# Kernel tuning notes

Hardware: AMD Instinct MI355X
Metric: run time of the kernel (lower is better)

The kernel has to match this reference:

```python
import jax, jax.numpy as jnp
import numpy as np

N_NODES = 51200      # 128 graphs * 400 ROIs
N_ROI = 400
HID = 64             # 'batch_size' arg of the torch module = hidden channels = n_timepoints
N_EDGES = 1638400    # avg degree 32
N_CLASSES = 2
NEG_SLOPE = 0.01


def setup_inputs():
    key = jax.random.key(0)
    ks = jax.random.split(key, 20)
    s = 0.05
    inp = {
        'x': jax.random.normal(ks[0], (N_NODES, HID), dtype=jnp.float32),
        'edge_index': jax.random.randint(ks[1], (2, N_EDGES), 0, N_NODES, dtype=jnp.int64),
        'edge_weight': jax.random.uniform(ks[2], (N_EDGES,), dtype=jnp.float32),
        # GCNConv weights stored [in, out]; biases [out]
        'W1': jax.random.normal(ks[3], (HID, HID), dtype=jnp.float32) * s,
        'b1': jnp.zeros((HID,), jnp.float32),
        'W2': jax.random.normal(ks[4], (HID, HID), dtype=jnp.float32) * s,
        'b2': jnp.zeros((HID,), jnp.float32),
        'W3': jax.random.normal(ks[5], (HID, HID), dtype=jnp.float32) * s,
        'b3': jnp.zeros((HID,), jnp.float32),
        'W4': jax.random.normal(ks[6], (HID, HID), dtype=jnp.float32) * s,
        'b4': jnp.zeros((HID,), jnp.float32),
        'fc1_w': jax.random.normal(ks[7], (N_ROI * HID, 256), dtype=jnp.float32) * 0.01,
        'fc1_b': jnp.zeros((256,), jnp.float32),
        'fc2_w': jax.random.normal(ks[8], (256, 128), dtype=jnp.float32) * s,
        'fc2_b': jnp.zeros((128,), jnp.float32),
        'fc3_w': jax.random.normal(ks[9], (128, N_CLASSES), dtype=jnp.float32) * s,
        'fc3_b': jnp.zeros((N_CLASSES,), jnp.float32),
    }
    return inp


def _gcn_norm(edge_index, edge_weight, n):
    # PyG GCNConv: add self-loops (weight 1), symmetric D^-1/2 A D^-1/2 normalization
    loop = jnp.arange(n, dtype=edge_index.dtype)
    src = jnp.concatenate([edge_index[0], loop])
    dst = jnp.concatenate([edge_index[1], loop])
    w = jnp.concatenate([edge_weight, jnp.ones((n,), edge_weight.dtype)])
    deg = jax.ops.segment_sum(w, dst, num_segments=n)
    dis = jnp.where(deg > 0, jax.lax.rsqrt(jnp.maximum(deg, 1e-30)), 0.0)
    norm = dis[src] * w * dis[dst]
    return src, dst, norm


def _conv(h, W, b, src, dst, norm, n):
    h = h @ W                                   # [N, out]
    msg = h[src] * norm[:, None]                # gather + scale
    out = jax.ops.segment_sum(msg, dst, num_segments=n) + b
    return out


def _leaky(v):
    return jnp.where(v >= 0, v, NEG_SLOPE * v)


def _head(h, fc1_w, fc1_b, fc2_w, fc2_b, fc3_w, fc3_b):
    # global_mean_pool with batch = arange(N) is identity; pool == reshape to graphs
    g = h.reshape(-1, N_ROI * HID)              # [G, n_roi*hid]
    g = g @ fc1_w + fc1_b                       # dropout is eval-mode identity
    g = g @ fc2_w + fc2_b
    g = g @ fc3_w + fc3_b
    return g


def reference(x, edge_index, edge_weight, W1, b1, W2, b2, W3, b3, W4, b4,
              fc1_w, fc1_b, fc2_w, fc2_b, fc3_w, fc3_b):
    n = x.shape[0]
    src, dst, norm = _gcn_norm(edge_index, edge_weight, n)
    h = _leaky(_conv(x, W1, b1, src, dst, norm, n))
    h = _leaky(_conv(h, W2, b2, src, dst, norm, n))
    h = _leaky(_conv(h, W3, b3, src, dst, norm, n))
    h = _leaky(_conv(h, W4, b4, src, dst, norm, n))
    logits = _head(h, fc1_w, fc1_b, fc2_w, fc2_b, fc3_w, fc3_b)
    logits0 = _head(x, fc1_w, fc1_b, fc2_w, fc2_b, fc3_w, fc3_b)
    penal = 0.09 * logits.shape[0] / jnp.linalg.norm(logits - logits0)
    return logits, penal
```

## Files before the change

kernel.cpp:

```cpp
#include <hip/hip_runtime.h>
#include <cstddef>

#define N_NODES 51200
#define N_EDGES 1638400
#define HID 64
#define N_ROI 400
#define N_GRAPHS 128
#define KHEAD 25600
#define NEG_SLOPE 0.01f
#define CAP 80
#define NCHUNK 400
#define CHUNK 4096
#define NBIN 512
#define BINSZ 100
#define LSTRIDE 81

typedef unsigned short u16;
typedef unsigned int u32;
typedef unsigned char u8;
typedef float f32x2 __attribute__((ext_vector_type(2)));

__device__ inline u16 f2bf(float f) {
    u32 u = __float_as_uint(f);
    u32 r = u + 0x7FFFu + ((u >> 16) & 1u);
    return (u16)(r >> 16);
}
__device__ inline float bf2f(u16 h) { return __uint_as_float(((u32)h) << 16); }

__device__ inline f32x2 dec8lo(u32 v) { return __builtin_amdgcn_cvt_pk_f32_fp8((int)v, false); }
__device__ inline f32x2 dec8hi(u32 v) { return __builtin_amdgcn_cvt_pk_f32_fp8((int)v, true); }
template <bool HI>
__device__ inline u32 enc8(float a, float b, u32 old) {
    return (u32)__builtin_amdgcn_cvt_pk_fp8_f32(a, b, (int)old, HI);
}
__device__ inline u32 pack4_fp8(float a, float b, float c, float d) {
    u32 w = enc8<false>(a, b, 0u);
    return enc8<true>(c, d, w);
}


__global__ __launch_bounds__(1024) void k1(const int* __restrict__ ei,
                                           const float* __restrict__ ew,
                                           uint2* __restrict__ chunkData,
                                           u32* __restrict__ offcnt,
                                           const float* __restrict__ x,
                                           u8* __restrict__ x8,
                                           const float* __restrict__ fc2w,
                                           const float* __restrict__ fc3w,
                                           const float* __restrict__ fc1b,
                                           const float* __restrict__ fc2b,
                                           const float* __restrict__ fc3b,
                                           float* __restrict__ fc23,
                                           float* __restrict__ bc) {
    int bid = blockIdx.x, t = threadIdx.x;
    __shared__ u32 cnt[NBIN];
    __shared__ u32 scan[NBIN];
    __shared__ u32 cur[NBIN];
    __shared__ uint2 stag[CHUNK];
    __shared__ float t1[128];

    if (bid < NCHUNK) {
        if (t < NBIN) cnt[t] = 0;
        __syncthreads();
        int base = bid * CHUNK;
        u32 lo[4]; float wv[4]; int bin[4];
        #pragma unroll
        for (int i = 0; i < 4; i++) {
            int e = base + i * 1024 + t;
            int s = ei[e], d = ei[N_EDGES + e];
            wv[i] = ew[e];
            bin[i] = d / BINSZ;
            lo[i] = (u32)s | ((u32)(d - bin[i] * BINSZ) << 16);
            atomicAdd(&cnt[bin[i]], 1u);
        }
        __syncthreads();
        if (t < NBIN) scan[t] = cnt[t];
        __syncthreads();
        for (int off = 1; off < NBIN; off <<= 1) {
            u32 add = (t < NBIN && t >= off) ? scan[t - off] : 0u;
            __syncthreads();
            if (t < NBIN) scan[t] += add;
            __syncthreads();
        }
        if (t < NBIN) cur[t] = scan[t] - cnt[t];
        __syncthreads();
        if (t < NBIN) offcnt[(size_t)bid * NBIN + t] = cur[t] | (cnt[t] << 16);
        __syncthreads();
        #pragma unroll
        for (int i = 0; i < 4; i++) {
            u32 pos = atomicAdd(&cur[bin[i]], 1u);
            stag[pos] = make_uint2(lo[i], __float_as_uint(wv[i]));
        }
        __syncthreads();
        #pragma unroll
        for (int i = 0; i < 4; i++)
            chunkData[base + i * 1024 + t] = stag[i * 1024 + t];
    } else if (bid < 600) {
        int idx = (bid - NCHUNK) * 1024 + t;
        const float4* xp = reinterpret_cast<const float4*>(x) + (size_t)idx * 4;
        float4 a = xp[0], b = xp[1], c = xp[2], d = xp[3];
        reinterpret_cast<uint4*>(x8)[idx] =
            make_uint4(pack4_fp8(a.x, a.y, a.z, a.w), pack4_fp8(b.x, b.y, b.z, b.w),
                       pack4_fp8(c.x, c.y, c.z, c.w), pack4_fp8(d.x, d.y, d.z, d.w));
    } else {
        if (t < 256) {
            float s0 = 0.f, s1 = 0.f;
            const float* row = fc2w + t * 128;
            for (int j = 0; j < 128; j++) {
                float a = row[j];
                s0 += a * fc3w[2 * j];
                s1 += a * fc3w[2 * j + 1];
            }
            fc23[2 * t] = s0;
            fc23[2 * t + 1] = s1;
        }
        if (t < 128) {
            float s = fc2b[t];
            for (int k = 0; k < 256; k++) s += fc1b[k] * fc2w[k * 128 + t];
            t1[t] = s;
        }
        __syncthreads();
        if (t < 2) {
            float s = fc3b[t];
            for (int j = 0; j < 128; j++) s += t1[j] * fc3w[2 * j + t];
            bc[t] = s;
        }
    }
}


__global__ __launch_bounds__(256) void k1t(const u32* __restrict__ in,
                                           u32* __restrict__ outT) {
    __shared__ u32 tile[32][33];
    int cx = blockIdx.x % 13, by = blockIdx.x / 13;
    int c0 = cx * 32, b0 = by * 32;
    int tx = threadIdx.x & 31, ty = threadIdx.x >> 5;
    for (int i = ty; i < 32; i += 8) {
        int c = c0 + i;
        if (c < NCHUNK) tile[i][tx] = in[(size_t)c * NBIN + b0 + tx];
    }
    __syncthreads();
    for (int i = ty; i < 32; i += 8) {
        int b = b0 + i;
        int c = c0 + tx;
        if (c < NCHUNK) outT[(size_t)b * NCHUNK + c] = tile[tx][i];
    }
}


__global__ __launch_bounds__(512) void k2(const uint2* __restrict__ chunkData,
                                          const u32* __restrict__ offcntT,
                                          u32* __restrict__ buck,
                                          int* __restrict__ cnts,
                                          float* __restrict__ dis,
                                          const float* __restrict__ fc1w,
                                          const float* __restrict__ fc23,
                                          float* __restrict__ Wc) {
    int bid = blockIdx.x, t = threadIdx.x;
    __shared__ u32 lbuck[BINSZ * LSTRIDE];
    __shared__ u32 lcnt[BINSZ];
    __shared__ float ldeg[BINSZ];
    __shared__ u32 oc[NCHUNK];

    if (bid < NBIN) {
        if (t < BINSZ) { lcnt[t] = 0; ldeg[t] = 0.f; }
        if (t < NCHUNK) oc[t] = offcntT[(size_t)bid * NCHUNK + t];
        __syncthreads();
        int w = t >> 6, lane = t & 63;
        int sBase = w * 50;
        for (int j = 0; j < 56; j += 8) {
            int s = sBase + j + (lane >> 3);
            int i0 = lane & 7;
            int k = 0, off = 0;
            if (j + (lane >> 3) < 50) {
                u32 o = oc[s];
                off = (int)(o & 0xffffu);
                k = (int)(o >> 16);
            }
            const uint2* cd = chunkData + (size_t)s * CHUNK + off;
            for (int i = i0; i < k; i += 8) {
                uint2 e = cd[i];
                u32 node = e.x >> 16;
                u32 src = e.x & 0xffffu;
                float ww = __uint_as_float(e.y);
                u32 pos = atomicAdd(&lcnt[node], 1u);
                if (pos < CAP - 1) lbuck[node * LSTRIDE + pos] = ((u32)f2bf(ww) << 16) | src;
                atomicAdd(&ldeg[node], ww);
            }
        }
        __syncthreads();
        int sg = t >> 5, ln = t & 31;
        for (int n = sg; n < BINSZ; n += 16) {
            int node = bid * BINSZ + n;
            int k = min((int)lcnt[n], CAP - 1);
            u32* dst = buck + (size_t)node * CAP;
            for (int i = ln; i < k; i += 32) dst[i] = lbuck[n * LSTRIDE + i];
            if (ln == 0) {
                cnts[node] = k;
                dis[node] = rsqrtf(1.f + ldeg[n]);
            }
        }
    } else {
        float* f23 = (float*)lbuck;
        f23[t] = fc23[t];
        __syncthreads();
        int r = (bid - NBIN) * 512 + t;
        const float* row = fc1w + (size_t)r * 256;
        float s0 = 0.f, s1 = 0.f;
        #pragma unroll 8
        for (int k = 0; k < 256; k++) {
            float a = row[k];
            s0 += a * f23[2 * k];
            s1 += a * f23[2 * k + 1];
        }
        Wc[2 * r] = s0;
        Wc[2 * r + 1] = s1;
    }
}


__global__ __launch_bounds__(1024) void k3(u32* __restrict__ buck,
                                           int* __restrict__ cnts,
                                           const float* __restrict__ dis) {
    int gt = blockIdx.x * 1024 + threadIdx.x;
    int node = gt >> 5, sub = gt & 31;
    float d = dis[node];
    int k = cnts[node];
    u32* bk = buck + (size_t)node * CAP;
    for (int j = sub; j < k; j += 32) {
        u32 e = bk[j];
        float val = bf2f((u16)(e >> 16)) * d * dis[e & 0xffffu];
        bk[j] = ((u32)f2bf(val) << 16) | (e & 0xffffu);
    }
    if (sub == 0) {
        bk[k] = ((u32)f2bf(d * d) << 16) | (u32)node;
        cnts[node] = k + 1;
    }
}


__global__ __launch_bounds__(512) void k_layer(const u8* __restrict__ H8,
                                               const u32* __restrict__ buck,
                                               const int* __restrict__ cnts,
                                               const float* __restrict__ W,
                                               const float* __restrict__ bias,
                                               u8* __restrict__ Hout) {
    __shared__ float Ws[64][64];
    __shared__ float ZsT[64][33];
    int t = threadIdx.x;
    int base = blockIdx.x * 32;

    #pragma unroll
    for (int i = 0; i < 2; i++) {
        int f = t + i * 512;
        int kk = f >> 4, c4 = f & 15;
        float4 wv = reinterpret_cast<const float4*>(W)[f];
        *reinterpret_cast<float4*>(&Ws[kk][c4 * 4]) = wv;
    }

    int grp = t >> 4, sub = t & 15;
    int node = base + grp;
    int k = cnts[node];
    const u32* bk = buck + (size_t)node * CAP;
    const u8* Hb = H8 + sub * 4;
    float a0 = 0.f, a1 = 0.f, a2 = 0.f, a3 = 0.f;
    for (int j0 = 0; j0 < k; j0 += 16) {
        int idx = j0 + sub;
        u32 pre = (idx < k) ? bk[idx] : 0u;
        #pragma unroll
        for (int i = 0; i < 16; i++) {
            u32 e = (u32)__shfl((int)pre, i, 16);
            float val = __uint_as_float(e & 0xffff0000u);
            u32 src = e & 0xffffu;
            u32 r = *reinterpret_cast<const u32*>(Hb + (size_t)src * HID);
            f32x2 lo = dec8lo(r), hi = dec8hi(r);
            a0 += val * lo.x; a1 += val * lo.y;
            a2 += val * hi.x; a3 += val * hi.y;
        }
    }
    ZsT[4 * sub + 0][grp] = a0;
    ZsT[4 * sub + 1][grp] = a1;
    ZsT[4 * sub + 2][grp] = a2;
    ZsT[4 * sub + 3][grp] = a3;
    __syncthreads();

    int r = t >> 4, c4 = t & 15;
    float4 acc = {0.f, 0.f, 0.f, 0.f};
    #pragma unroll 8
    for (int kk = 0; kk < 64; kk++) {
        float a = ZsT[kk][r];
        const float4 w = *reinterpret_cast<const float4*>(&Ws[kk][c4 * 4]);
        acc.x += a * w.x; acc.y += a * w.y; acc.z += a * w.z; acc.w += a * w.w;
    }
    float4 bb = reinterpret_cast<const float4*>(bias)[c4];
    float v0 = acc.x + bb.x, v1 = acc.y + bb.y, v2 = acc.z + bb.z, v3 = acc.w + bb.w;
    v0 = v0 >= 0.f ? v0 : NEG_SLOPE * v0;
    v1 = v1 >= 0.f ? v1 : NEG_SLOPE * v1;
    v2 = v2 >= 0.f ? v2 : NEG_SLOPE * v2;
    v3 = v3 >= 0.f ? v3 : NEG_SLOPE * v3;
    *reinterpret_cast<u32*>(Hout + (size_t)(base + r) * HID + c4 * 4) =
        pack4_fp8(v0, v1, v2, v3);
}


__global__ __launch_bounds__(256) void k_logits(const u8* __restrict__ h4,
                                                const float* __restrict__ x,
                                                const float* __restrict__ Wc,
                                                const float* __restrict__ bc,
                                                float* __restrict__ out,
                                                float* __restrict__ sq,
                                                int* __restrict__ done) {
    int g = blockIdx.x, t = threadIdx.x;
    const u8* bh = h4 + (size_t)g * KHEAD;
    const float* bx = x + (size_t)g * KHEAD;
    float aH0 = 0.f, aH1 = 0.f, aX0 = 0.f, aX1 = 0.f;
    for (int k2 = t; k2 < KHEAD / 2; k2 += 256) {
        u32 hv = reinterpret_cast<const u16*>(bh)[k2];
        f32x2 h = dec8lo(hv);
        float2 xv = reinterpret_cast<const float2*>(bx)[k2];
        float4 wc = reinterpret_cast<const float4*>(Wc)[k2];
        aH0 += h.x * wc.x + h.y * wc.z;
        aH1 += h.x * wc.y + h.y * wc.w;
        aX0 += xv.x * wc.x + xv.y * wc.z;
        aX1 += xv.x * wc.y + xv.y * wc.w;
    }
    for (int off = 32; off > 0; off >>= 1) {
        aH0 += __shfl_down(aH0, off);
        aH1 += __shfl_down(aH1, off);
        aX0 += __shfl_down(aX0, off);
        aX1 += __shfl_down(aX1, off);
    }
    __shared__ float red[4][4];
    int wave = t >> 6, lane = t & 63;
    if (lane == 0) {
        red[wave][0] = aH0; red[wave][1] = aH1;
        red[wave][2] = aX0; red[wave][3] = aX1;
    }
    __syncthreads();
    if (t == 0) {
        float h0 = red[0][0] + red[1][0] + red[2][0] + red[3][0];
        float h1 = red[0][1] + red[1][1] + red[2][1] + red[3][1];
        float x0 = red[0][2] + red[1][2] + red[2][2] + red[3][2];
        float x1 = red[0][3] + red[1][3] + red[2][3] + red[3][3];
        out[2 * g]     = h0 + bc[0];
        out[2 * g + 1] = h1 + bc[1];
        float d0 = h0 - x0, d1 = h1 - x1;
        atomicAdd(sq, d0 * d0 + d1 * d1);
        __threadfence();
        int c = atomicAdd(done, 1);
        if (c == N_GRAPHS - 1) {
            __threadfence();
            float s = atomicAdd(sq, 0.f);
            out[2 * N_GRAPHS] = 0.09f * (float)N_GRAPHS / sqrtf(s);
        }
    }
}


extern "C" void kernel_launch(void* const* d_in, const int* in_sizes, int n_in,
                              void* d_out, int out_size, void* d_ws, size_t ws_size,
                              hipStream_t stream) {
    const float* x    = (const float*)d_in[0];
    const int*   ei   = (const int*)d_in[1];
    const float* ew   = (const float*)d_in[2];
    const float* W1   = (const float*)d_in[3];
    const float* b1   = (const float*)d_in[4];
    const float* W2   = (const float*)d_in[5];
    const float* b2   = (const float*)d_in[6];
    const float* W3   = (const float*)d_in[7];
    const float* b3   = (const float*)d_in[8];
    const float* W4   = (const float*)d_in[9];
    const float* b4   = (const float*)d_in[10];
    const float* fc1w = (const float*)d_in[11];
    const float* fc1b = (const float*)d_in[12];
    const float* fc2w = (const float*)d_in[13];
    const float* fc2b = (const float*)d_in[14];
    const float* fc3w = (const float*)d_in[15];
    const float* fc3b = (const float*)d_in[16];
    float* out = (float*)d_out;

    char* base = (char*)d_ws;
    size_t off = 0;
    auto alloc = [&](size_t bytes) -> void* {
        void* p = base + off;
        off += (bytes + 255) & ~(size_t)255;
        return p;
    };
    uint2* chunkData = (uint2*)alloc((size_t)N_EDGES * 8);
    u32*   offcnt    = (u32*)alloc((size_t)NCHUNK * NBIN * 4);
    u32*   offcntT   = (u32*)alloc((size_t)NCHUNK * NBIN * 4);
    u32*   buck      = (u32*)alloc((size_t)N_NODES * CAP * 4);
    int*   cnts      = (int*)alloc((size_t)N_NODES * 4);
    float* dis       = (float*)alloc((size_t)N_NODES * 4);
    u8*    x8        = (u8*)alloc((size_t)N_NODES * HID);
    u8*    ha        = (u8*)alloc((size_t)N_NODES * HID);
    u8*    hb        = (u8*)alloc((size_t)N_NODES * HID);
    float* fc23      = (float*)alloc(512 * 4);
    float* bc        = (float*)alloc(2 * 4);
    float* Wc        = (float*)alloc((size_t)KHEAD * 2 * 4);
    char*  ctrl      = (char*)alloc(256);
    float* sq        = (float*)ctrl;
    int*   done      = (int*)(ctrl + 4);

    (void)hipMemsetAsync(ctrl, 0, 8, stream);
    k1<<<601, 1024, 0, stream>>>(ei, ew, chunkData, offcnt, x, x8,
                                 fc2w, fc3w, fc1b, fc2b, fc3b, fc23, bc);
    k1t<<<13 * 16, 256, 0, stream>>>(offcnt, offcntT);
    k2<<<NBIN + 50, 512, 0, stream>>>(chunkData, offcntT, buck, cnts, dis,
                                      fc1w, fc23, Wc);
    k3<<<1600, 1024, 0, stream>>>(buck, cnts, dis);

    const float* Wl[4] = {W1, W2, W3, W4};
    const float* bl[4] = {b1, b2, b3, b4};
    u8* hbufs[2] = {ha, hb};
    const u8* hin = x8;
    for (int l = 0; l < 4; l++) {
        u8* hout = hbufs[l & 1];
        k_layer<<<N_NODES / 32, 512, 0, stream>>>(hin, buck, cnts,
                                                  Wl[l], bl[l], hout);
        hin = hout;
    }

    k_logits<<<N_GRAPHS, 256, 0, stream>>>(hin, x, Wc, bc, out, sq, done);
}
```

Measured before the change: 192.1 us.

## Fold edge normalization into layer kernel, vectorize binning, and retile GEMM

Removes the k3 normalization pass: each layer now applies dis[src] and dis[dst] on the fly and handles the self-loop from the node's own features. Chunk size doubles with vectorized int4/float4 edge loads, and the per-chunk scan now uses wave shuffles instead of a barrier-heavy Hillis-Steele loop. The layer kernel processes 64 nodes per 1024-thread block with a 4x4 register-tiled 64x64 GEMM run by 256 threads. The trade-off is one extra dis gather per edge in each of the four layers, and idle threads during the GEMM phase.

```diff
diff --git a/kernel.cpp b/kernel.cpp
--- a/kernel.cpp
+++ b/kernel.cpp
@@ -9,8 +9,8 @@
 #define KHEAD 25600
 #define NEG_SLOPE 0.01f
 #define CAP 80
-#define NCHUNK 400
-#define CHUNK 4096
+#define NCHUNK 200
+#define CHUNK 8192
 #define NBIN 512
 #define BINSZ 100
 #define LSTRIDE 81
@@ -54,8 +54,8 @@
                                            float* __restrict__ bc) {
     int bid = blockIdx.x, t = threadIdx.x;
     __shared__ u32 cnt[NBIN];
-    __shared__ u32 scan[NBIN];
     __shared__ u32 cur[NBIN];
+    __shared__ u32 wsum[8];
     __shared__ uint2 stag[CHUNK];
     __shared__ float t1[128];
 
@@ -63,39 +63,60 @@
         if (t < NBIN) cnt[t] = 0;
         __syncthreads();
         int base = bid * CHUNK;
-        u32 lo[4]; float wv[4]; int bin[4];
+        const int4* sp = reinterpret_cast<const int4*>(ei + base);
+        const int4* dp = reinterpret_cast<const int4*>(ei + N_EDGES + base);
+        const float4* wp = reinterpret_cast<const float4*>(ew + base);
+        int4 sa = sp[2 * t], sb = sp[2 * t + 1];
+        int4 da = dp[2 * t], db = dp[2 * t + 1];
+        float4 wa = wp[2 * t], wb = wp[2 * t + 1];
+        int ss[8] = {sa.x, sa.y, sa.z, sa.w, sb.x, sb.y, sb.z, sb.w};
+        int dd[8] = {da.x, da.y, da.z, da.w, db.x, db.y, db.z, db.w};
+        float wv[8] = {wa.x, wa.y, wa.z, wa.w, wb.x, wb.y, wb.z, wb.w};
+        u32 lo[8]; int bin[8];
         #pragma unroll
-        for (int i = 0; i < 4; i++) {
-            int e = base + i * 1024 + t;
-            int s = ei[e], d = ei[N_EDGES + e];
-            wv[i] = ew[e];
-            bin[i] = d / BINSZ;
-            lo[i] = (u32)s | ((u32)(d - bin[i] * BINSZ) << 16);
-            atomicAdd(&cnt[bin[i]], 1u);
-        }
-        __syncthreads();
-        if (t < NBIN) scan[t] = cnt[t];
-        __syncthreads();
-        for (int off = 1; off < NBIN; off <<= 1) {
-            u32 add = (t < NBIN && t >= off) ? scan[t - off] : 0u;
-            __syncthreads();
-            if (t < NBIN) scan[t] += add;
-            __syncthreads();
-        }
-        if (t < NBIN) cur[t] = scan[t] - cnt[t];
-        __syncthreads();
-        if (t < NBIN) offcnt[(size_t)bid * NBIN + t] = cur[t] | (cnt[t] << 16);
+        for (int i = 0; i < 8; i++) {
+            int b = dd[i] / BINSZ;
+            bin[i] = b;
+            lo[i] = (u32)ss[i] | ((u32)(dd[i] - b * BINSZ) << 16);
+            atomicAdd(&cnt[b], 1u);
+        }
+        __syncthreads();
+        int wave = t >> 6, lane = t & 63;
+        u32 v = 0, inc = 0;
+        if (t < NBIN) {
+            v = cnt[t];
+            inc = v;
+            #pragma unroll
+            for (int d = 1; d < 64; d <<= 1) {
+                u32 o = __shfl_up(inc, d, 64);
+                if (lane >= d) inc += o;
+            }
+            if (lane == 63) wsum[wave] = inc;
+        }
+        __syncthreads();
+        if (t == 0) {
+            u32 r = 0;
+            #pragma unroll
+            for (int i = 0; i < 8; i++) { u32 c = wsum[i]; wsum[i] = r; r += c; }
+        }
+        __syncthreads();
+        if (t < NBIN) {
+            u32 excl = inc - v + wsum[wave];
+            cur[t] = excl;
+            offcnt[(size_t)bid * NBIN + t] = excl | (v << 16);
+        }
         __syncthreads();
         #pragma unroll
-        for (int i = 0; i < 4; i++) {
+        for (int i = 0; i < 8; i++) {
             u32 pos = atomicAdd(&cur[bin[i]], 1u);
             stag[pos] = make_uint2(lo[i], __float_as_uint(wv[i]));
         }
         __syncthreads();
+        const uint4* sg4 = reinterpret_cast<const uint4*>(stag);
+        uint4* out4 = reinterpret_cast<uint4*>(chunkData + (size_t)base);
         #pragma unroll
-        for (int i = 0; i < 4; i++)
-            chunkData[base + i * 1024 + t] = stag[i * 1024 + t];
-    } else if (bid < 600) {
+        for (int i = 0; i < 4; i++) out4[i * 1024 + t] = sg4[i * 1024 + t];
+    } else if (bid < 400) {
         int idx = (bid - NCHUNK) * 1024 + t;
         const float4* xp = reinterpret_cast<const float4*>(x) + (size_t)idx * 4;
         float4 a = xp[0], b = xp[1], c = xp[2], d = xp[3];
@@ -132,8 +153,8 @@
 __global__ __launch_bounds__(256) void k1t(const u32* __restrict__ in,
                                            u32* __restrict__ outT) {
     __shared__ u32 tile[32][33];
-    int cx = blockIdx.x % 13, by = blockIdx.x / 13;
-    int c0 = cx * 32, b0 = by * 32;
+    int bx = blockIdx.x & 15, cy = blockIdx.x >> 4;
+    int b0 = bx * 32, c0 = cy * 32;
     int tx = threadIdx.x & 31, ty = threadIdx.x >> 5;
     for (int i = ty; i < 32; i += 8) {
         int c = c0 + i;
@@ -167,12 +188,13 @@
         if (t < NCHUNK) oc[t] = offcntT[(size_t)bid * NCHUNK + t];
         __syncthreads();
         int w = t >> 6, lane = t & 63;
-        int sBase = w * 50;
-        for (int j = 0; j < 56; j += 8) {
-            int s = sBase + j + (lane >> 3);
+        int sBase = w * 25;
+        for (int j = 0; j < 32; j += 8) {
+            int so = j + (lane >> 3);
+            int s = sBase + so;
             int i0 = lane & 7;
             int k = 0, off = 0;
-            if (j + (lane >> 3) < 50) {
+            if (so < 25) {
                 u32 o = oc[s];
                 off = (int)(o & 0xffffu);
                 k = (int)(o >> 16);
@@ -219,87 +241,81 @@
 }
 
 
-__global__ __launch_bounds__(1024) void k3(u32* __restrict__ buck,
-                                           int* __restrict__ cnts,
-                                           const float* __restrict__ dis) {
-    int gt = blockIdx.x * 1024 + threadIdx.x;
-    int node = gt >> 5, sub = gt & 31;
-    float d = dis[node];
-    int k = cnts[node];
-    u32* bk = buck + (size_t)node * CAP;
-    for (int j = sub; j < k; j += 32) {
-        u32 e = bk[j];
-        float val = bf2f((u16)(e >> 16)) * d * dis[e & 0xffffu];
-        bk[j] = ((u32)f2bf(val) << 16) | (e & 0xffffu);
-    }
-    if (sub == 0) {
-        bk[k] = ((u32)f2bf(d * d) << 16) | (u32)node;
-        cnts[node] = k + 1;
-    }
-}
-
-
-__global__ __launch_bounds__(512) void k_layer(const u8* __restrict__ H8,
-                                               const u32* __restrict__ buck,
-                                               const int* __restrict__ cnts,
-                                               const float* __restrict__ W,
-                                               const float* __restrict__ bias,
-                                               u8* __restrict__ Hout) {
+__global__ __launch_bounds__(1024) void k_layer(const u8* __restrict__ H8,
+                                                const u32* __restrict__ buck,
+                                                const int* __restrict__ cnts,
+                                                const float* __restrict__ dis,
+                                                const float* __restrict__ W,
+                                                const float* __restrict__ bias,
+                                                u8* __restrict__ Hout) {
     __shared__ float Ws[64][64];
-    __shared__ float ZsT[64][33];
+    __shared__ float ZsT[64][72];
     int t = threadIdx.x;
-    int base = blockIdx.x * 32;
-
-    #pragma unroll
-    for (int i = 0; i < 2; i++) {
-        int f = t + i * 512;
-        int kk = f >> 4, c4 = f & 15;
-        float4 wv = reinterpret_cast<const float4*>(W)[f];
+    int base = blockIdx.x * 64;
+
+    {
+        int kk = t >> 4, c4 = t & 15;
+        float4 wv = reinterpret_cast<const float4*>(W)[t];
         *reinterpret_cast<float4*>(&Ws[kk][c4 * 4]) = wv;
     }
 
     int grp = t >> 4, sub = t & 15;
     int node = base + grp;
     int k = cnts[node];
+    float d = dis[node];
+    const u32* H32 = reinterpret_cast<const u32*>(H8);
     const u32* bk = buck + (size_t)node * CAP;
-    const u8* Hb = H8 + sub * 4;
-    float a0 = 0.f, a1 = 0.f, a2 = 0.f, a3 = 0.f;
+    u32 own = H32[node * 16 + sub];
+    f32x2 olo = dec8lo(own), ohi = dec8hi(own);
+    float a0 = d * olo.x, a1 = d * olo.y, a2 = d * ohi.x, a3 = d * ohi.y;
     for (int j0 = 0; j0 < k; j0 += 16) {
         int idx = j0 + sub;
-        u32 pre = (idx < k) ? bk[idx] : 0u;
+        u32 pre = 0; float pd = 0.f;
+        if (idx < k) { pre = bk[idx]; pd = dis[pre & 0xffffu]; }
         #pragma unroll
         for (int i = 0; i < 16; i++) {
             u32 e = (u32)__shfl((int)pre, i, 16);
-            float val = __uint_as_float(e & 0xffff0000u);
+            float ds = __shfl(pd, i, 16);
+            float val = __uint_as_float(e & 0xffff0000u) * ds;
             u32 src = e & 0xffffu;
-            u32 r = *reinterpret_cast<const u32*>(Hb + (size_t)src * HID);
+            u32 r = H32[src * 16 + sub];
             f32x2 lo = dec8lo(r), hi = dec8hi(r);
             a0 += val * lo.x; a1 += val * lo.y;
             a2 += val * hi.x; a3 += val * hi.y;
         }
     }
-    ZsT[4 * sub + 0][grp] = a0;
-    ZsT[4 * sub + 1][grp] = a1;
-    ZsT[4 * sub + 2][grp] = a2;
-    ZsT[4 * sub + 3][grp] = a3;
+    ZsT[4 * sub + 0][grp] = d * a0;
+    ZsT[4 * sub + 1][grp] = d * a1;
+    ZsT[4 * sub + 2][grp] = d * a2;
+    ZsT[4 * sub + 3][grp] = d * a3;
     __syncthreads();
 
-    int r = t >> 4, c4 = t & 15;
-    float4 acc = {0.f, 0.f, 0.f, 0.f};
-    #pragma unroll 8
-    for (int kk = 0; kk < 64; kk++) {
-        float a = ZsT[kk][r];
-        const float4 w = *reinterpret_cast<const float4*>(&Ws[kk][c4 * 4]);
-        acc.x += a * w.x; acc.y += a * w.y; acc.z += a * w.z; acc.w += a * w.w;
-    }
-    float4 bb = reinterpret_cast<const float4*>(bias)[c4];
-    float v0 = acc.x + bb.x, v1 = acc.y + bb.y, v2 = acc.z + bb.z, v3 = acc.w + bb.w;
-    v0 = v0 >= 0.f ? v0 : NEG_SLOPE * v0;
-    v1 = v1 >= 0.f ? v1 : NEG_SLOPE * v1;
-    v2 = v2 >= 0.f ? v2 : NEG_SLOPE * v2;
-    v3 = v3 >= 0.f ? v3 : NEG_SLOPE * v3;
-    *reinterpret_cast<u32*>(Hout + (size_t)(base + r) * HID + c4 * 4) =
-        pack4_fp8(v0, v1, v2, v3);
+    if (t < 256) {
+        int r0 = (t >> 4) * 4, c0 = (t & 15) * 4;
+        float4 acc0 = {0,0,0,0}, acc1 = {0,0,0,0}, acc2 = {0,0,0,0}, acc3 = {0,0,0,0};
+        #pragma unroll 4
+        for (int kk = 0; kk < 64; kk++) {
+            float4 z = *reinterpret_cast<const float4*>(&ZsT[kk][r0]);
+            float4 w = *reinterpret_cast<const float4*>(&Ws[kk][c0]);
+            acc0.x += z.x * w.x; acc0.y += z.x * w.y; acc0.z += z.x * w.z; acc0.w += z.x * w.w;
+            acc1.x += z.y * w.x; acc1.y += z.y * w.y; acc1.z += z.y * w.z; acc1.w += z.y * w.w;
+            acc2.x += z.z * w.x; acc2.y += z.z * w.y; acc2.z += z.z * w.z; acc2.w += z.z * w.w;
+            acc3.x += z.w * w.x; acc3.y += z.w * w.y; acc3.z += z.w * w.z; acc3.w += z.w * w.w;
+        }
+        float4 bb = *reinterpret_cast<const float4*>(bias + c0);
+        u32* outp = reinterpret_cast<u32*>(Hout);
+        float4 accs[4] = {acc0, acc1, acc2, acc3};
+        #pragma unroll
+        for (int j = 0; j < 4; j++) {
+            float v0 = accs[j].x + bb.x, v1 = accs[j].y + bb.y;
+            float v2 = accs[j].z + bb.z, v3 = accs[j].w + bb.w;
+            v0 = v0 >= 0.f ? v0 : NEG_SLOPE * v0;
+            v1 = v1 >= 0.f ? v1 : NEG_SLOPE * v1;
+            v2 = v2 >= 0.f ? v2 : NEG_SLOPE * v2;
+            v3 = v3 >= 0.f ? v3 : NEG_SLOPE * v3;
+            outp[(size_t)(base + r0 + j) * 16 + (c0 >> 2)] = pack4_fp8(v0, v1, v2, v3);
+        }
+    }
 }
 
 
@@ -403,12 +419,11 @@
     int*   done      = (int*)(ctrl + 4);
 
     (void)hipMemsetAsync(ctrl, 0, 8, stream);
-    k1<<<601, 1024, 0, stream>>>(ei, ew, chunkData, offcnt, x, x8,
+    k1<<<401, 1024, 0, stream>>>(ei, ew, chunkData, offcnt, x, x8,
                                  fc2w, fc3w, fc1b, fc2b, fc3b, fc23, bc);
-    k1t<<<13 * 16, 256, 0, stream>>>(offcnt, offcntT);
+    k1t<<<112, 256, 0, stream>>>(offcnt, offcntT);
     k2<<<NBIN + 50, 512, 0, stream>>>(chunkData, offcntT, buck, cnts, dis,
                                       fc1w, fc23, Wc);
-    k3<<<1600, 1024, 0, stream>>>(buck, cnts, dis);
 
     const float* Wl[4] = {W1, W2, W3, W4};
     const float* bl[4] = {b1, b2, b3, b4};
@@ -416,8 +431,8 @@
     const u8* hin = x8;
     for (int l = 0; l < 4; l++) {
         u8* hout = hbufs[l & 1];
-        k_layer<<<N_NODES / 32, 512, 0, stream>>>(hin, buck, cnts,
-                                                  Wl[l], bl[l], hout);
+        k_layer<<<N_NODES / 64, 1024, 0, stream>>>(hin, buck, cnts, dis,
+                                                   Wl[l], bl[l], hout);
         hin = hout;
     }
 
```

Measured after the change: 215.6 us. 1.12x slower.
